# Optimization experiments

Measured on AMD Instinct MI355X. Metric: run time of the kernel, lower is better.

The kernel has to match this reference:

```python
import jax, jax.numpy as jnp
import numpy as np

N_LIG, N_REC = 4096, 16384
E_LIG, E_REC = 65536, 262144
H, OUT, ORIG = 256, 256, 64
EF_LIG, EF_REC = 16, 16
N_SIG = 15
SLOPE = 0.01      # leakyrelu_neg_slope
SKIP_H = 0.5      # skip_weight_h
X_INIT = 0.25     # x_connection_init
SIGMAS = np.asarray(1.5 ** np.arange(N_SIG), dtype=np.float32)  # all_sigmas_dist


def _lrelu(x):
    return jax.nn.leaky_relu(x, SLOPE)


def _mlp2(x, w1, b1, w2, b2):
    # Linear -> LeakyReLU -> (Identity norm) -> Linear
    return _lrelu(x @ w1 + b1) @ w2 + b2


def _seg_mean(vals, idx, n):
    s = jax.ops.segment_sum(vals, idx, num_segments=n)
    d = jax.ops.segment_sum(jnp.ones((vals.shape[0], 1), vals.dtype), idx, num_segments=n)
    return s / jnp.maximum(d, 1.0)


def _rbf(x_rel):
    # multi-sigma RBF of squared edge distance: exp(-|x_rel|^2 / sigma), 15 sigmas
    d2 = jnp.sum(x_rel * x_rel, axis=1, keepdims=True)        # [E,1]
    return jnp.exp(-d2 / jnp.asarray(SIGMAS, x_rel.dtype))    # [E,15]


def _cross_attention(q, k, v, mask):
    a = mask * (q @ k.T) - 1000.0 * (1.0 - mask)
    return jax.nn.softmax(a, axis=1) @ v


def setup_inputs():
    key = jax.random.key(0)
    ks = iter(jax.random.split(key, 64))

    def rn(*shape):
        return jax.random.normal(next(ks), shape, dtype=jnp.float32)

    def w(fi, fo):
        return rn(fi, fo) / np.float32(np.sqrt(fi))

    e_in_l = 2 * H + EF_LIG + N_SIG
    e_in_r = 2 * H + EF_REC + N_SIG
    n_in = ORIG + H + OUT
    z = lambda d: jnp.zeros((d,), jnp.float32)
    inp = dict(
        coords_lig=rn(N_LIG, 3), h_feats_lig=rn(N_LIG, H),
        orig_lig_feats=rn(N_LIG, ORIG), orig_coords_lig=rn(N_LIG, 3),
        coords_rec=rn(N_REC, 3), h_feats_rec=rn(N_REC, H),
        orig_rec_feats=rn(N_REC, ORIG), orig_coords_rec=rn(N_REC, 3),
        mask=jnp.ones((N_LIG, N_REC), jnp.float32),
        lig_edge_feat=rn(E_LIG, EF_LIG), rec_edge_feat=rn(E_REC, EF_REC),
        lig_src=jax.random.randint(next(ks), (E_LIG,), 0, N_LIG),
        lig_dst=jax.random.randint(next(ks), (E_LIG,), 0, N_LIG),
        rec_src=jax.random.randint(next(ks), (E_REC,), 0, N_REC),
        rec_dst=jax.random.randint(next(ks), (E_REC,), 0, N_REC),
        lig_edge_w1=w(e_in_l, OUT), lig_edge_b1=z(OUT), lig_edge_w2=w(OUT, OUT), lig_edge_b2=z(OUT),
        rec_edge_w1=w(e_in_r, OUT), rec_edge_b1=z(OUT), rec_edge_w2=w(OUT, OUT), rec_edge_b2=z(OUT),
        att_q_lig_w=w(H, H), att_k_lig_w=w(H, H), att_v_lig_w=w(H, H),
        att_q_rec_w=w(H, H), att_k_rec_w=w(H, H), att_v_rec_w=w(H, H),
        node_lig_w1=w(n_in, H), node_lig_b1=z(H), node_lig_w2=w(H, OUT), node_lig_b2=z(OUT),
        node_rec_w1=w(n_in, H), node_rec_b1=z(H), node_rec_w2=w(H, OUT), node_rec_b2=z(OUT),
        coords_lig_w1=w(OUT, OUT), coords_lig_b1=z(OUT), coords_lig_w2=w(OUT, 1), coords_lig_b2=z(1),
        coords_rec_w1=w(OUT, OUT), coords_rec_b1=z(OUT), coords_rec_w2=w(OUT, 1), coords_rec_b2=z(1),
    )
    return inp


def reference(coords_lig, h_feats_lig, orig_lig_feats, orig_coords_lig,
              coords_rec, h_feats_rec, orig_rec_feats, orig_coords_rec,
              mask, lig_edge_feat, rec_edge_feat,
              lig_src, lig_dst, rec_src, rec_dst,
              lig_edge_w1, lig_edge_b1, lig_edge_w2, lig_edge_b2,
              rec_edge_w1, rec_edge_b1, rec_edge_w2, rec_edge_b2,
              att_q_lig_w, att_k_lig_w, att_v_lig_w,
              att_q_rec_w, att_k_rec_w, att_v_rec_w,
              node_lig_w1, node_lig_b1, node_lig_w2, node_lig_b2,
              node_rec_w1, node_rec_b1, node_rec_w2, node_rec_b2,
              coords_lig_w1, coords_lig_b1, coords_lig_w2, coords_lig_b2,
              coords_rec_w1, coords_rec_b1, coords_rec_w2, coords_rec_b2):
    n_lig, n_rec = coords_lig.shape[0], coords_rec.shape[0]
    # edge messages: gather endpoint features + edge attrs + RBF(dist)
    x_rel_l = coords_lig[lig_src] - coords_lig[lig_dst]                       # [E_lig,3]
    msg_l = _mlp2(jnp.concatenate([h_feats_lig[lig_src], h_feats_lig[lig_dst],
                                   lig_edge_feat, _rbf(x_rel_l)], axis=1),
                  lig_edge_w1, lig_edge_b1, lig_edge_w2, lig_edge_b2)         # [E_lig,OUT]
    x_rel_r = coords_rec[rec_src] - coords_rec[rec_dst]
    msg_r = _mlp2(jnp.concatenate([h_feats_rec[rec_src], h_feats_rec[rec_dst],
                                   rec_edge_feat, _rbf(x_rel_r)], axis=1),
                  rec_edge_w1, rec_edge_b1, rec_edge_w2, rec_edge_b2)         # [E_rec,OUT]
    # cross attention between ligand and receptor node sets
    cross_l = _cross_attention(_lrelu(h_feats_lig @ att_q_lig_w),
                               _lrelu(h_feats_rec @ att_k_rec_w),
                               h_feats_rec @ att_v_rec_w, mask)               # [N_lig,H]
    cross_r = _cross_attention(_lrelu(h_feats_rec @ att_q_rec_w),
                               _lrelu(h_feats_lig @ att_k_lig_w),
                               h_feats_lig @ att_v_lig_w, mask.T)             # [N_rec,H]
    # equivariant coordinate updates: mean over incoming edges of x_rel * coords_mlp(msg)
    x_upd_l = _seg_mean(x_rel_l * _mlp2(msg_l, coords_lig_w1, coords_lig_b1,
                                        coords_lig_w2, coords_lig_b2), lig_dst, n_lig)
    x_upd_r = _seg_mean(x_rel_r * _mlp2(msg_r, coords_rec_w1, coords_rec_b1,
                                        coords_rec_w2, coords_rec_b2), rec_dst, n_rec)
    x_ev_l = X_INIT * orig_coords_lig + (1.0 - X_INIT) * coords_lig + x_upd_l
    x_ev_r = X_INIT * orig_coords_rec + (1.0 - X_INIT) * coords_rec + x_upd_r
    # node feature updates: cat(aggr_msg, cross_att, original features) -> MLP + skip
    aggr_l = _seg_mean(msg_l, lig_dst, n_lig)
    aggr_r = _seg_mean(msg_r, rec_dst, n_rec)
    h_l = SKIP_H * _mlp2(jnp.concatenate([aggr_l, cross_l, orig_lig_feats], axis=1),
                         node_lig_w1, node_lig_b1, node_lig_w2, node_lig_b2) \
          + (1.0 - SKIP_H) * h_feats_lig
    h_r = SKIP_H * _mlp2(jnp.concatenate([aggr_r, cross_r, orig_rec_feats], axis=1),
                         node_rec_w1, node_rec_b1, node_rec_w2, node_rec_b2) \
          + (1.0 - SKIP_H) * h_feats_rec
    return (x_ev_l, h_l, x_ev_r, h_r)
```

## Files before the change

### kernel.cpp

```cpp
#include <hip/hip_runtime.h>
#include <hip/hip_bf16.h>


#define N_LIG   4096
#define N_REC   16384
#define E_LIG_N 65536
#define E_REC_N 262144
#define HD      256
#define ORIGD   64
#define EFD     16
#define NSIG    15
#define EIN     543
#define XP      552
#define XPN     584
#define XPP     264
#define FP      264

typedef __bf16 bf16x8 __attribute__((ext_vector_type(8)));
typedef float  f32x4  __attribute__((ext_vector_type(4)));

__device__ __forceinline__ float lrelu(float x) { return x > 0.f ? x : 0.01f * x; }
__device__ __forceinline__ unsigned short f2bu(float f) {
    __hip_bfloat16 h = __float2bfloat16(f);
    return *reinterpret_cast<unsigned short*>(&h);
}

__device__ __forceinline__ void glds16(const void* g, void* l) {
    __builtin_amdgcn_global_load_lds(
        (const __attribute__((address_space(1))) void*)g,
        (__attribute__((address_space(3))) void*)l,
        16, 0, 0);
}

__device__ __forceinline__ void stage_tile(
    const __hip_bfloat16* g, unsigned short* l, int wave, int lane)
{
    #pragma unroll
    for (int i = 0; i < 2; ++i) {
        const __hip_bfloat16* gp = g + (size_t)(i * 512 + wave * 64 + lane) * 8;
        unsigned short* lp = l + (i * 512 + wave * 64) * 8;
        glds16(gp, lp);
    }
}

__device__ __forceinline__ void mfma_gemm(
    const unsigned short* sA, int pitch,
    const __hip_bfloat16* Wswz, int KS, int lane, f32x4 acc[2][4])
{
    const int col = lane & 15, quad = lane >> 4;
    const unsigned short* a0p = sA + (size_t)col * pitch + quad * 8;
    const unsigned short* a1p = sA + (size_t)(16 + col) * pitch + quad * 8;
    const __hip_bfloat16* wp = Wswz + lane * 8;
    bf16x8 bc[4], bn[4], a0c, a1c, a0n, a1n;
    #pragma unroll
    for (int nt = 0; nt < 4; ++nt)
        bc[nt] = *reinterpret_cast<const bf16x8*>(wp + (size_t)nt * KS * 512);
    a0c = *reinterpret_cast<const bf16x8*>(a0p);
    a1c = *reinterpret_cast<const bf16x8*>(a1p);
    for (int ks = 0; ks < KS; ++ks) {
        if (ks + 1 < KS) {
            #pragma unroll
            for (int nt = 0; nt < 4; ++nt)
                bn[nt] = *reinterpret_cast<const bf16x8*>(
                    wp + ((size_t)nt * KS + ks + 1) * 512);
            a0n = *reinterpret_cast<const bf16x8*>(a0p + (ks + 1) * 32);
            a1n = *reinterpret_cast<const bf16x8*>(a1p + (ks + 1) * 32);
        }
        #pragma unroll
        for (int nt = 0; nt < 4; ++nt) {
            acc[0][nt] = __builtin_amdgcn_mfma_f32_16x16x32_bf16(a0c, bc[nt], acc[0][nt], 0, 0, 0);
            acc[1][nt] = __builtin_amdgcn_mfma_f32_16x16x32_bf16(a1c, bc[nt], acc[1][nt], 0, 0, 0);
        }
        #pragma unroll
        for (int nt = 0; nt < 4; ++nt) bc[nt] = bn[nt];
        a0c = a0n; a1c = a1n;
    }
}

__global__ void zero_kernel(float* __restrict__ p, int n) {
    int i = blockIdx.x * 256 + threadIdx.x;
    if (i < n) p[i] = 0.f;
}

__global__ void f2b_kernel(const float* __restrict__ src,
                           __hip_bfloat16* __restrict__ dst, int n8) {
    const int i = blockIdx.x * 256 + threadIdx.x;
    if (i >= n8) return;
    const float4 a = *reinterpret_cast<const float4*>(src + (size_t)i * 8);
    const float4 b = *reinterpret_cast<const float4*>(src + (size_t)i * 8 + 4);
    ushort4 u0 = { f2bu(a.x), f2bu(a.y), f2bu(a.z), f2bu(a.w) };
    ushort4 u1 = { f2bu(b.x), f2bu(b.y), f2bu(b.z), f2bu(b.w) };
    unsigned short* d = (unsigned short*)dst + (size_t)i * 8;
    *reinterpret_cast<ushort4*>(d)     = u0;
    *reinterpret_cast<ushort4*>(d + 4) = u1;
}

__global__ void hist_kernel(const int* __restrict__ dst, int* __restrict__ hist, int n) {
    int i = blockIdx.x * 256 + threadIdx.x;
    if (i < n) atomicAdd(&hist[dst[i]], 1);
}

__global__ __launch_bounds__(256) void scan_kernel(
    const int* __restrict__ hist, int* __restrict__ cur,
    float* __restrict__ cntf, int n)
{
    __shared__ int part[256];
    const int tid = threadIdx.x;
    const int per = n >> 8;
    const int base = tid * per;
    int s = 0;
    for (int i = 0; i < per; ++i) s += hist[base + i];
    part[tid] = s;
    __syncthreads();
    #pragma unroll
    for (int off = 1; off < 256; off <<= 1) {
        int v = (tid >= off) ? part[tid - off] : 0;
        __syncthreads();
        part[tid] += v;
        __syncthreads();
    }
    int run = part[tid] - s;
    for (int i = 0; i < per; ++i) {
        const int h = hist[base + i];
        cur[base + i]  = run;
        cntf[base + i] = (float)h;
        run += h;
    }
}

__global__ void scatter_kernel(const int* __restrict__ dst, int* __restrict__ cur,
                               int* __restrict__ elist, int n) {
    int i = blockIdx.x * 256 + threadIdx.x;
    if (i < n) { int p = atomicAdd(&cur[dst[i]], 1); elist[p] = i; }
}

__global__ void wt_swz(const float* __restrict__ src,
                       __hip_bfloat16* __restrict__ dst, int K, int KS) {
    const int g  = blockIdx.x / KS;
    const int ks = blockIdx.x % KS;
    for (int i = threadIdx.x; i < 512; i += 256) {
        const int lane = i >> 3, j = i & 7;
        const int n = g * 16 + (lane & 15);
        const int k = ks * 32 + (lane >> 4) * 8 + j;
        const float v = (k < K) ? src[(size_t)k * 256 + n] : 0.f;
        dst[((size_t)(g * KS + ks) * 64 + lane) * 8 + j] = __float2bfloat16(v);
    }
}

__global__ __launch_bounds__(256) void kswz_kernel(
    const __hip_bfloat16* __restrict__ K, __hip_bfloat16* __restrict__ blob)
{
    const int c = blockIdx.x * 256 + threadIdx.x;
    const int lane = c & 63;
    const int s    = (c >> 6) & 7;
    const int kt   = c >> 9;
    const __hip_bfloat16* src =
        K + (size_t)(kt * 16 + (lane & 15)) * HD + s * 32 + (lane >> 4) * 8;
    *reinterpret_cast<uint4*>(blob + (size_t)c * 8) =
        *reinterpret_cast<const uint4*>(src);
}

__global__ __launch_bounds__(256) void vswz_kernel(
    const __hip_bfloat16* __restrict__ V, __hip_bfloat16* __restrict__ blob)
{
    __shared__ unsigned short s[32][264];
    const int jt  = blockIdx.x;
    const int tid = threadIdx.x;
    {
        const int row = tid >> 3;
        const int d0  = (tid & 7) * 32;
        const __hip_bfloat16* vp = V + (size_t)(jt * 32 + row) * HD + d0;
        #pragma unroll
        for (int i = 0; i < 4; ++i)
            *reinterpret_cast<uint4*>(&s[row][d0 + 8 * i]) =
                *reinterpret_cast<const uint4*>(vp + 8 * i);
    }
    __syncthreads();
    {
        const int w    = tid >> 6;
        const int lane = tid & 63;
        const int col  = lane & 15;
        const int quad = lane >> 4;
        #pragma unroll
        for (int i = 0; i < 4; ++i) {
            const int dt = w + i * 4;
            unsigned short tmp[8];
            #pragma unroll
            for (int j = 0; j < 8; ++j)
                tmp[j] = s[quad * 8 + j][dt * 16 + col];
            *reinterpret_cast<uint4*>(
                blob + ((size_t)(jt * 16 + dt) * 64 + lane) * 8) =
                *reinterpret_cast<uint4*>(tmp);
        }
    }
}

__global__ __launch_bounds__(256, 4) void edge_mfma(
    const float* __restrict__ coords, const __hip_bfloat16* __restrict__ hb,
    const __hip_bfloat16* __restrict__ efb,
    const int* __restrict__ src, const int* __restrict__ dst,
    const int* __restrict__ elist,
    const __hip_bfloat16* __restrict__ W1s, const float* __restrict__ b1,
    const __hip_bfloat16* __restrict__ W2s, const float* __restrict__ b2,
    const __hip_bfloat16* __restrict__ Wc1s, const float* __restrict__ bc1,
    const float* __restrict__ wc2v, const float* __restrict__ bc2,
    float* __restrict__ aggr, float* __restrict__ xsum)
{
    __shared__ unsigned short sX[32][XP];
    __shared__ float sXrel[32][3];
    __shared__ int   sDst[32];
    __shared__ int   sSrc[32];
    __shared__ int   sE[32];
    __shared__ float sRedW[4][32];
    __shared__ float sPv[32];

    const int tid  = threadIdx.x;
    const int lane = tid & 63;
    const int wave = tid >> 6;
    const int col  = lane & 15;
    const int quad = lane >> 4;
    const int e0   = blockIdx.x * 32;

    if (tid < 32) {
        const int e = elist[e0 + tid];
        const int s = src[e], d = dst[e];
        sE[tid] = e; sSrc[tid] = s; sDst[tid] = d;
        float d2 = 0.f;
        #pragma unroll
        for (int c = 0; c < 3; ++c) {
            const float xr = coords[s * 3 + c] - coords[d * 3 + c];
            sXrel[tid][c] = xr;
            d2 += xr * xr;
        }
        float sig = 1.0f;
        #pragma unroll
        for (int si = 0; si < NSIG; ++si) {
            sX[tid][528 + si] = f2bu(__expf(-d2 / sig));
            sig *= 1.5f;
        }
        sX[tid][543] = 0;
    }
    __syncthreads();

    for (int i = tid; i < 32 * 64; i += 256) {
        const int row = i >> 6, c = i & 63;
        const int node = (c < 32) ? sSrc[row] : sDst[row];
        const int chunk = c & 31;
        *reinterpret_cast<uint4*>(&sX[row][(c < 32 ? 0 : 256) + chunk * 8]) =
            *reinterpret_cast<const uint4*>(&hb[(size_t)node * HD + chunk * 8]);
    }
    if (tid < 64) {
        const int row = tid >> 1, hh = tid & 1;
        *reinterpret_cast<uint4*>(&sX[row][512 + hh * 8]) =
            *reinterpret_cast<const uint4*>(&efb[(size_t)sE[row] * EFD + hh * 8]);
    }
    __syncthreads();

    f32x4 acc[2][4];
    f32x4 macc[2][4];

    #pragma unroll
    for (int nt = 0; nt < 4; ++nt) {
        const float bv = b1[wave * 64 + nt * 16 + col];
        acc[0][nt] = { bv, bv, bv, bv };
        acc[1][nt] = { bv, bv, bv, bv };
    }
    mfma_gemm(&sX[0][0], XP, W1s + (size_t)(wave * 4) * 17 * 512, 17, lane, acc);
    __syncthreads();
    #pragma unroll
    for (int mt = 0; mt < 2; ++mt)
        #pragma unroll
        for (int nt = 0; nt < 4; ++nt)
            #pragma unroll
            for (int r = 0; r < 4; ++r)
                sX[mt * 16 + quad * 4 + r][wave * 64 + nt * 16 + col] =
                    f2bu(lrelu(acc[mt][nt][r]));
    __syncthreads();

    #pragma unroll
    for (int nt = 0; nt < 4; ++nt) {
        const float bv = b2[wave * 64 + nt * 16 + col];
        macc[0][nt] = { bv, bv, bv, bv };
        macc[1][nt] = { bv, bv, bv, bv };
    }
    mfma_gemm(&sX[0][0], XP, W2s + (size_t)(wave * 4) * 8 * 512, 8, lane, macc);
    __syncthreads();
    #pragma unroll
    for (int mt = 0; mt < 2; ++mt)
        #pragma unroll
        for (int nt = 0; nt < 4; ++nt)
            #pragma unroll
            for (int r = 0; r < 4; ++r)
                sX[mt * 16 + quad * 4 + r][wave * 64 + nt * 16 + col] =
                    f2bu(macc[mt][nt][r]);
    __syncthreads();

    #pragma unroll
    for (int nt = 0; nt < 4; ++nt) {
        const float bv = bc1[wave * 64 + nt * 16 + col];
        acc[0][nt] = { bv, bv, bv, bv };
        acc[1][nt] = { bv, bv, bv, bv };
    }
    mfma_gemm(&sX[0][0], XP, Wc1s + (size_t)(wave * 4) * 8 * 512, 8, lane, acc);
    float w2l[4];
    #pragma unroll
    for (int nt = 0; nt < 4; ++nt) w2l[nt] = wc2v[wave * 64 + nt * 16 + col];
    #pragma unroll
    for (int mt = 0; mt < 2; ++mt) {
        float pr[4] = { 0.f, 0.f, 0.f, 0.f };
        #pragma unroll
        for (int nt = 0; nt < 4; ++nt)
            #pragma unroll
            for (int r = 0; r < 4; ++r)
                pr[r] += lrelu(acc[mt][nt][r]) * w2l[nt];
        #pragma unroll
        for (int r = 0; r < 4; ++r) {
            #pragma unroll
            for (int off = 1; off < 16; off <<= 1) pr[r] += __shfl_xor(pr[r], off);
        }
        if (col == 0)
            #pragma unroll
            for (int r = 0; r < 4; ++r)
                sRedW[wave][mt * 16 + quad * 4 + r] = pr[r];
    }
    __syncthreads();

    float* sF = reinterpret_cast<float*>(&sX[0][0]);
    #pragma unroll
    for (int mt = 0; mt < 2; ++mt)
        #pragma unroll
        for (int nt = 0; nt < 4; ++nt)
            #pragma unroll
            for (int r = 0; r < 4; ++r)
                sF[(mt * 16 + quad * 4 + r) * FP + wave * 64 + nt * 16 + col] =
                    macc[mt][nt][r];
    if (tid < 32)
        sPv[tid] = sRedW[0][tid] + sRedW[1][tid] + sRedW[2][tid] + sRedW[3][tid]
                 + bc2[0];
    __syncthreads();

    {
        const int c = tid;
        float av = 0.f;
        int dprev = sDst[0];
        for (int row = 0; row < 32; ++row) {
            const int d = sDst[row];
            if (d != dprev) {
                atomicAdd(&aggr[(size_t)dprev * HD + c], av);
                av = 0.f; dprev = d;
            }
            av += sF[row * FP + c];
        }
        atomicAdd(&aggr[(size_t)dprev * HD + c], av);
    }
    if (tid < 3) {
        const int c = tid;
        float av = 0.f;
        int dprev = sDst[0];
        for (int row = 0; row < 32; ++row) {
            const int d = sDst[row];
            if (d != dprev) {
                atomicAdd(&xsum[(size_t)dprev * 3 + c], av);
                av = 0.f; dprev = d;
            }
            av += sXrel[row][c] * sPv[row];
        }
        atomicAdd(&xsum[(size_t)dprev * 3 + c], av);
    }
}

__global__ __launch_bounds__(256, 4) void node_mfma(
    const float* __restrict__ aggr, const float* __restrict__ cnt,
    const __hip_bfloat16* __restrict__ cross, const float* __restrict__ orig,
    const float* __restrict__ hfeat,
    const __hip_bfloat16* __restrict__ WN1s, const float* __restrict__ b1,
    const __hip_bfloat16* __restrict__ WN2s, const float* __restrict__ b2,
    float* __restrict__ out)
{
    __shared__ unsigned short sXn[32][XPN];
    __shared__ float sInv[32];

    const int tid  = threadIdx.x;
    const int lane = tid & 63;
    const int wave = tid >> 6;
    const int col  = lane & 15;
    const int quad = lane >> 4;
    const int r0   = blockIdx.x * 32;

    if (tid < 32) sInv[tid] = 1.f / fmaxf(cnt[r0 + tid], 1.f);
    __syncthreads();

    for (int i = tid; i < 32 * 64; i += 256) {
        const int row = i >> 6, c4 = i & 63;
        const float inv = sInv[row];
        const float4 v = *reinterpret_cast<const float4*>(
            &aggr[(size_t)(r0 + row) * HD + c4 * 4]);
        ushort4 u = { f2bu(v.x * inv), f2bu(v.y * inv), f2bu(v.z * inv), f2bu(v.w * inv) };
        *reinterpret_cast<ushort4*>(&sXn[row][c4 * 4]) = u;
    }
    for (int i = tid; i < 32 * 64; i += 256) {
        const int row = i >> 6, c4 = i & 63;
        const ushort4 u = *reinterpret_cast<const ushort4*>(
            &cross[(size_t)(r0 + row) * HD + c4 * 4]);
        *reinterpret_cast<ushort4*>(&sXn[row][256 + c4 * 4]) = u;
    }
    for (int i = tid; i < 32 * 16; i += 256) {
        const int row = i >> 4, c4 = i & 15;
        const float4 v = *reinterpret_cast<const float4*>(
            &orig[(size_t)(r0 + row) * ORIGD + c4 * 4]);
        ushort4 u = { f2bu(v.x), f2bu(v.y), f2bu(v.z), f2bu(v.w) };
        *reinterpret_cast<ushort4*>(&sXn[row][512 + c4 * 4]) = u;
    }
    __syncthreads();

    f32x4 acc[2][4];

    #pragma unroll
    for (int nt = 0; nt < 4; ++nt) {
        const float bv = b1[wave * 64 + nt * 16 + col];
        acc[0][nt] = { bv, bv, bv, bv };
        acc[1][nt] = { bv, bv, bv, bv };
    }
    mfma_gemm(&sXn[0][0], XPN, WN1s + (size_t)(wave * 4) * 18 * 512, 18, lane, acc);
    __syncthreads();
    #pragma unroll
    for (int mt = 0; mt < 2; ++mt)
        #pragma unroll
        for (int nt = 0; nt < 4; ++nt)
            #pragma unroll
            for (int r = 0; r < 4; ++r)
                sXn[mt * 16 + quad * 4 + r][wave * 64 + nt * 16 + col] =
                    f2bu(lrelu(acc[mt][nt][r]));
    __syncthreads();

    #pragma unroll
    for (int nt = 0; nt < 4; ++nt) {
        const float bv = b2[wave * 64 + nt * 16 + col];
        acc[0][nt] = { bv, bv, bv, bv };
        acc[1][nt] = { bv, bv, bv, bv };
    }
    mfma_gemm(&sXn[0][0], XPN, WN2s + (size_t)(wave * 4) * 8 * 512, 8, lane, acc);
    #pragma unroll
    for (int mt = 0; mt < 2; ++mt)
        #pragma unroll
        for (int nt = 0; nt < 4; ++nt)
            #pragma unroll
            for (int r = 0; r < 4; ++r) {
                const int g = r0 + mt * 16 + quad * 4 + r;
                const int n = wave * 64 + nt * 16 + col;
                out[(size_t)g * HD + n] =
                    0.5f * acc[mt][nt][r] + 0.5f * hfeat[(size_t)g * HD + n];
            }
}

__global__ __launch_bounds__(256, 4) void qkv_proj(
    const __hip_bfloat16* __restrict__ Xb,
    const __hip_bfloat16* __restrict__ Wq, const __hip_bfloat16* __restrict__ Wk,
    const __hip_bfloat16* __restrict__ Wv,
    __hip_bfloat16* __restrict__ Q, __hip_bfloat16* __restrict__ K,
    __hip_bfloat16* __restrict__ V)
{
    __shared__ unsigned short sXp[32][XPP];
    const int tid  = threadIdx.x;
    const int lane = tid & 63;
    const int wave = tid >> 6;
    const int col  = lane & 15;
    const int quad = lane >> 4;
    const int r0   = blockIdx.x * 32;

    for (int i = tid; i < 32 * 32; i += 256) {
        const int row = i >> 5, c = i & 31;
        *reinterpret_cast<uint4*>(&sXp[row][c * 8]) =
            *reinterpret_cast<const uint4*>(&Xb[(size_t)(r0 + row) * HD + c * 8]);
    }
    __syncthreads();

    f32x4 acc[2][4];
    #pragma unroll
    for (int p = 0; p < 3; ++p) {
        const __hip_bfloat16* Ws = (p == 0) ? Wq : (p == 1) ? Wk : Wv;
        __hip_bfloat16* outp     = (p == 0) ? Q  : (p == 1) ? K  : V;
        #pragma unroll
        for (int nt = 0; nt < 4; ++nt) {
            acc[0][nt] = { 0.f, 0.f, 0.f, 0.f };
            acc[1][nt] = { 0.f, 0.f, 0.f, 0.f };
        }
        mfma_gemm(&sXp[0][0], XPP, Ws + (size_t)(wave * 4) * 8 * 512, 8, lane, acc);
        #pragma unroll
        for (int mt = 0; mt < 2; ++mt)
            #pragma unroll
            for (int nt = 0; nt < 4; ++nt)
                #pragma unroll
                for (int r = 0; r < 4; ++r) {
                    float v = acc[mt][nt][r];
                    if (p < 2) v = lrelu(v);
                    outp[(size_t)(r0 + mt * 16 + quad * 4 + r) * HD +
                         wave * 64 + nt * 16 + col] = __float2bfloat16(v);
                }
    }
}

__device__ __forceinline__ void load_mask(
    const float* __restrict__ maskG, int transposed, int R0, int j0,
    int wave, int quad, int col, float mv[2][4])
{
    if (!transposed) {
        #pragma unroll
        for (int t = 0; t < 2; ++t)
            #pragma unroll
            for (int r = 0; r < 4; ++r)
                mv[t][r] = maskG[(size_t)(R0 + wave * 16 + quad * 4 + r) * N_REC
                                 + j0 + col + 16 * t];
    } else {
        #pragma unroll
        for (int t = 0; t < 2; ++t)
            #pragma unroll
            for (int r = 0; r < 4; ++r)
                mv[t][r] = maskG[(size_t)(j0 + col + 16 * t) * N_REC
                                 + R0 + wave * 16 + quad * 4 + r];
    }
}

__device__ __forceinline__ void attn_tile(
    const unsigned short* sK, const unsigned short* sV,
    unsigned short (*sPw)[40], const bf16x8 qf[8], const float mv[2][4],
    int lane, int col, int quad, f32x4 o[16], float m[4], float l[4])
{
    f32x4 sacc[2];
    sacc[0][0]=0.f; sacc[0][1]=0.f; sacc[0][2]=0.f; sacc[0][3]=0.f;
    sacc[1][0]=0.f; sacc[1][1]=0.f; sacc[1][2]=0.f; sacc[1][3]=0.f;
    #pragma unroll
    for (int t = 0; t < 2; ++t) {
        #pragma unroll
        for (int s = 0; s < 8; ++s) {
            bf16x8 kf = *reinterpret_cast<const bf16x8*>(
                &sK[(t * 8 + s) * 512 + lane * 8]);
            sacc[t] = __builtin_amdgcn_mfma_f32_16x16x32_bf16(qf[s], kf, sacc[t], 0, 0, 0);
        }
    }

    float a[2][4];
    #pragma unroll
    for (int t = 0; t < 2; ++t)
        #pragma unroll
        for (int r = 0; r < 4; ++r)
            a[t][r] = mv[t][r] * sacc[t][r] - 1000.f * (1.f - mv[t][r]);

    float lm[4];
    #pragma unroll
    for (int r = 0; r < 4; ++r) lm[r] = fmaxf(a[0][r], a[1][r]);
    float w = lm[0] - m[0];
    #pragma unroll
    for (int r = 1; r < 4; ++r) w = fmaxf(w, lm[r] - m[r]);
    if (!__all(w <= 8.f)) {
        #pragma unroll
        for (int r = 0; r < 4; ++r) {
            float mx = lm[r];
            #pragma unroll
            for (int off = 1; off < 16; off <<= 1)
                mx = fmaxf(mx, __shfl_xor(mx, off));
            const float mn = fmaxf(m[r], mx);
            const float c  = __expf(m[r] - mn);
            m[r] = mn;
            l[r] *= c;
            #pragma unroll
            for (int dt = 0; dt < 16; ++dt) o[dt][r] *= c;
        }
    }

    #pragma unroll
    for (int r = 0; r < 4; ++r) {
        const float p0 = __expf(a[0][r] - m[r]);
        const float p1 = __expf(a[1][r] - m[r]);
        sPw[quad * 4 + r][col]      = f2bu(p0);
        sPw[quad * 4 + r][col + 16] = f2bu(p1);
        l[r] += p0 + p1;
    }

    bf16x8 pf = *reinterpret_cast<const bf16x8*>(&sPw[col][quad * 8]);
    #pragma unroll
    for (int dt = 0; dt < 16; ++dt) {
        bf16x8 vf = *reinterpret_cast<const bf16x8*>(&sV[dt * 512 + lane * 8]);
        o[dt] = __builtin_amdgcn_mfma_f32_16x16x32_bf16(pf, vf, o[dt], 0, 0, 0);
    }
}

__global__ __launch_bounds__(512) void attn_mfma(
    const __hip_bfloat16* __restrict__ Qb, const __hip_bfloat16* __restrict__ Kz,
    const __hip_bfloat16* __restrict__ Vz, const float* __restrict__ maskG,
    float* __restrict__ PO, float* __restrict__ PM, float* __restrict__ PL,
    int M, int chunkKeys, int transposed)
{
    __shared__ unsigned short sKb[2][8192];
    __shared__ unsigned short sVb[2][8192];
    __shared__ unsigned short sP[8][16][40];

    const int tid  = threadIdx.x;
    const int lane = tid & 63;
    const int wave = tid >> 6;
    const int col  = lane & 15;
    const int quad = lane >> 4;
    const int R0   = blockIdx.x * 128;
    const int split = blockIdx.y;
    const int jbase = split * chunkKeys;

    bf16x8 qf[8];
    {
        const __hip_bfloat16* qp =
            Qb + (size_t)(R0 + wave * 16 + col) * HD + quad * 8;
        #pragma unroll
        for (int s = 0; s < 8; ++s)
            qf[s] = *reinterpret_cast<const bf16x8*>(qp + 32 * s);
    }

    f32x4 o[16];
    #pragma unroll
    for (int dt = 0; dt < 16; ++dt) { o[dt][0]=0.f; o[dt][1]=0.f; o[dt][2]=0.f; o[dt][3]=0.f; }
    float m[4], l[4];
    #pragma unroll
    for (int r = 0; r < 4; ++r) { m[r] = -INFINITY; l[r] = 0.f; }

    float mvA[2][4], mvB[2][4];

    stage_tile(Kz + (size_t)jbase * 256, &sKb[0][0], wave, lane);
    stage_tile(Vz + (size_t)jbase * 256, &sVb[0][0], wave, lane);
    load_mask(maskG, transposed, R0, jbase, wave, quad, col, mvA);

    for (int jt = 0; jt < chunkKeys; jt += 64) {
        asm volatile("s_waitcnt vmcnt(0)" ::: "memory");
        __builtin_amdgcn_s_barrier();
        __builtin_amdgcn_sched_barrier(0);
        stage_tile(Kz + (size_t)(jbase + jt + 32) * 256, &sKb[1][0], wave, lane);
        stage_tile(Vz + (size_t)(jbase + jt + 32) * 256, &sVb[1][0], wave, lane);
        load_mask(maskG, transposed, R0, jbase + jt + 32, wave, quad, col, mvB);
        __builtin_amdgcn_sched_barrier(0);
        attn_tile(&sKb[0][0], &sVb[0][0], sP[wave], qf, mvA,
                  lane, col, quad, o, m, l);

        asm volatile("s_waitcnt vmcnt(0)" ::: "memory");
        __builtin_amdgcn_s_barrier();
        __builtin_amdgcn_sched_barrier(0);
        if (jt + 64 < chunkKeys) {
            stage_tile(Kz + (size_t)(jbase + jt + 64) * 256, &sKb[0][0], wave, lane);
            stage_tile(Vz + (size_t)(jbase + jt + 64) * 256, &sVb[0][0], wave, lane);
            load_mask(maskG, transposed, R0, jbase + jt + 64, wave, quad, col, mvA);
        }
        __builtin_amdgcn_sched_barrier(0);
        attn_tile(&sKb[1][0], &sVb[1][0], sP[wave], qf, mvB,
                  lane, col, quad, o, m, l);
    }

    #pragma unroll
    for (int r = 0; r < 4; ++r) {
        #pragma unroll
        for (int off = 1; off < 16; off <<= 1)
            l[r] += __shfl_xor(l[r], off);
    }

    #pragma unroll
    for (int dt = 0; dt < 16; ++dt)
        #pragma unroll
        for (int r = 0; r < 4; ++r) {
            const int row = R0 + wave * 16 + quad * 4 + r;
            PO[((size_t)split * M + row) * HD + dt * 16 + col] = o[dt][r];
        }
    if (col == 0) {
        #pragma unroll
        for (int r = 0; r < 4; ++r) {
            const int row = R0 + wave * 16 + quad * 4 + r;
            PM[(size_t)split * M + row] = m[r];
            PL[(size_t)split * M + row] = l[r];
        }
    }
}

__global__ void attn_combine(
    const float* __restrict__ PO, const float* __restrict__ PM,
    const float* __restrict__ PL, __hip_bfloat16* __restrict__ Out,
    int M, int nchunks)
{
    const int idx = blockIdx.x * 256 + threadIdx.x;
    const int row = idx >> 8;
    float mmax = -INFINITY;
    for (int c = 0; c < nchunks; ++c) mmax = fmaxf(mmax, PM[(size_t)c * M + row]);
    float denom = 0.f, acc = 0.f;
    for (int c = 0; c < nchunks; ++c) {
        const float w = __expf(PM[(size_t)c * M + row] - mmax);
        denom += PL[(size_t)c * M + row] * w;
        acc   += PO[(size_t)c * M * HD + idx] * w;
    }
    Out[idx] = __float2bfloat16(acc / denom);
}

__global__ void coords_fin(
    const float* __restrict__ coords, const float* __restrict__ origc,
    const float* __restrict__ xsum, const float* __restrict__ cnt,
    float* __restrict__ out, int n)
{
    const int i = blockIdx.x * 256 + threadIdx.x;
    if (i >= n * 3) return;
    const int node = i / 3;
    const float inv = 1.f / fmaxf(cnt[node], 1.f);
    out[i] = 0.25f * origc[i] + 0.75f * coords[i] + xsum[i] * inv;
}

extern "C" void kernel_launch(void* const* d_in, const int* in_sizes, int n_in,
                              void* d_out, int out_size, void* d_ws, size_t ws_size,
                              hipStream_t stream)
{
    const float* coords_lig = (const float*)d_in[0];
    const float* h_lig      = (const float*)d_in[1];
    const float* orig_lig   = (const float*)d_in[2];
    const float* origc_lig  = (const float*)d_in[3];
    const float* coords_rec = (const float*)d_in[4];
    const float* h_rec      = (const float*)d_in[5];
    const float* orig_rec   = (const float*)d_in[6];
    const float* origc_rec  = (const float*)d_in[7];
    const float* mask       = (const float*)d_in[8];
    const float* lig_ef     = (const float*)d_in[9];
    const float* rec_ef     = (const float*)d_in[10];
    const int* lig_src = (const int*)d_in[11];
    const int* lig_dst = (const int*)d_in[12];
    const int* rec_src = (const int*)d_in[13];
    const int* rec_dst = (const int*)d_in[14];
    const float* le_w1 = (const float*)d_in[15];
    const float* le_b1 = (const float*)d_in[16];
    const float* le_w2 = (const float*)d_in[17];
    const float* le_b2 = (const float*)d_in[18];
    const float* re_w1 = (const float*)d_in[19];
    const float* re_b1 = (const float*)d_in[20];
    const float* re_w2 = (const float*)d_in[21];
    const float* re_b2 = (const float*)d_in[22];
    const float* aql_w = (const float*)d_in[23];
    const float* akl_w = (const float*)d_in[24];
    const float* avl_w = (const float*)d_in[25];
    const float* aqr_w = (const float*)d_in[26];
    const float* akr_w = (const float*)d_in[27];
    const float* avr_w = (const float*)d_in[28];
    const float* nl_w1 = (const float*)d_in[29];
    const float* nl_b1 = (const float*)d_in[30];
    const float* nl_w2 = (const float*)d_in[31];
    const float* nl_b2 = (const float*)d_in[32];
    const float* nr_w1 = (const float*)d_in[33];
    const float* nr_b1 = (const float*)d_in[34];
    const float* nr_w2 = (const float*)d_in[35];
    const float* nr_b2 = (const float*)d_in[36];
    const float* cl_w1 = (const float*)d_in[37];
    const float* cl_b1 = (const float*)d_in[38];
    const float* cl_w2 = (const float*)d_in[39];
    const float* cl_b2 = (const float*)d_in[40];
    const float* cr_w1 = (const float*)d_in[41];
    const float* cr_b1 = (const float*)d_in[42];
    const float* cr_w2 = (const float*)d_in[43];
    const float* cr_b2 = (const float*)d_in[44];

    float* out = (float*)d_out;
    float* wsf = (float*)d_ws;

    const size_t AGGRL = 0;
    const size_t AGGRR = AGGRL + (size_t)N_LIG * HD;
    const size_t CNTL  = AGGRR + (size_t)N_REC * HD;
    const size_t CNTR  = CNTL + N_LIG;
    const size_t XSUML = CNTR + N_REC;
    const size_t XSUMR = XSUML + (size_t)N_LIG * 3;
    const size_t HISTL = XSUMR + (size_t)N_REC * 3;
    const size_t CURL  = HISTL + N_LIG;
    const size_t HISTR = CURL + N_LIG;
    const size_t CURR  = HISTR + N_REC;
    const size_t ZEND  = CURR + N_REC;
    const size_t ELISTL = ZEND;
    const size_t ELISTR = ELISTL + E_LIG_N;
    const size_t FEND   = ELISTR + E_REC_N;

    __hip_bfloat16* wsb = (__hip_bfloat16*)(wsf + FEND);
    const size_t QL  = 0;
    const size_t KL  = QL + (size_t)N_LIG * HD;
    const size_t VL  = KL + (size_t)N_LIG * HD;
    const size_t QR  = VL + (size_t)N_LIG * HD;
    const size_t KR  = QR + (size_t)N_REC * HD;
    const size_t VR  = KR + (size_t)N_REC * HD;
    const size_t CRL = VR + (size_t)N_REC * HD;
    const size_t CRR = CRL + (size_t)N_LIG * HD;
    const size_t KZL = CRR + (size_t)N_REC * HD;
    const size_t VZL = KZL + (size_t)N_LIG * HD;
    const size_t KZR = VZL + (size_t)N_LIG * HD;
    const size_t VZR = KZR + (size_t)N_REC * HD;
    const size_t EW1SZ = (size_t)16 * 17 * 512;
    const size_t KW256 = (size_t)16 * 8 * 512;
    const size_t NW1SZ = (size_t)16 * 18 * 512;
    const size_t SW_EL1 = VZR + (size_t)N_REC * HD;
    const size_t SW_EL2 = SW_EL1 + EW1SZ;
    const size_t SW_EC1 = SW_EL2 + KW256;
    const size_t SW_NL1 = SW_EC1 + KW256;
    const size_t SW_NL2 = SW_NL1 + NW1SZ;
    const size_t SW_ER1 = SW_NL2 + KW256;
    const size_t SW_ER2 = SW_ER1 + EW1SZ;
    const size_t SW_EC1R = SW_ER2 + KW256;
    const size_t SW_NR1 = SW_EC1R + KW256;
    const size_t SW_NR2 = SW_NR1 + NW1SZ;
    const size_t SW_PQL = SW_NR2 + KW256;
    const size_t SW_PKL = SW_PQL + KW256;
    const size_t SW_PVL = SW_PKL + KW256;
    const size_t SW_PQR = SW_PVL + KW256;
    const size_t SW_PKR = SW_PQR + KW256;
    const size_t SW_PVR = SW_PKR + KW256;
    const size_t HB_L  = SW_PVR + KW256;
    const size_t HB_R  = HB_L + (size_t)N_LIG * HD;
    const size_t EFB_L = HB_R + (size_t)N_REC * HD;
    const size_t EFB_R = EFB_L + (size_t)E_LIG_N * EFD;
    const size_t BF_END = EFB_R + (size_t)E_REC_N * EFD;

    float* wsp = (float*)(wsb + ((BF_END + 1) & ~(size_t)1));
    const size_t baseBytes = (size_t)((char*)wsp - (char*)d_ws);
    int SL = 16, SR = 4;
    {
        const size_t poElems16 = (size_t)16 * N_LIG * HD;
        const size_t need16 = baseBytes +
            (poElems16 + 2 * (size_t)16 * N_LIG) * sizeof(float);
        if (ws_size < need16) { SL = 8; SR = 2; }
    }
    const size_t PO_ = 0;
    const size_t PM_ = PO_ + (size_t)SL * N_LIG * HD;
    const size_t PL_ = PM_ + (size_t)SL * N_LIG;

    const size_t O_XL = 0;
    const size_t O_HL = O_XL + (size_t)N_LIG * 3;
    const size_t O_XR = O_HL + (size_t)N_LIG * HD;
    const size_t O_HR = O_XR + (size_t)N_REC * 3;

    zero_kernel<<<((int)ZEND + 255) / 256, 256, 0, stream>>>(wsf, (int)ZEND);

    f2b_kernel<<<(N_LIG * HD / 8 + 255) / 256, 256, 0, stream>>>(
        h_lig, wsb + HB_L, N_LIG * HD / 8);
    f2b_kernel<<<(N_REC * HD / 8 + 255) / 256, 256, 0, stream>>>(
        h_rec, wsb + HB_R, N_REC * HD / 8);
    f2b_kernel<<<(E_LIG_N * EFD / 8 + 255) / 256, 256, 0, stream>>>(
        lig_ef, wsb + EFB_L, E_LIG_N * EFD / 8);
    f2b_kernel<<<(E_REC_N * EFD / 8 + 255) / 256, 256, 0, stream>>>(
        rec_ef, wsb + EFB_R, E_REC_N * EFD / 8);

    hist_kernel<<<E_LIG_N / 256, 256, 0, stream>>>(lig_dst, (int*)(wsf + HISTL), E_LIG_N);
    hist_kernel<<<E_REC_N / 256, 256, 0, stream>>>(rec_dst, (int*)(wsf + HISTR), E_REC_N);
    scan_kernel<<<1, 256, 0, stream>>>((int*)(wsf + HISTL), (int*)(wsf + CURL),
                                       wsf + CNTL, N_LIG);
    scan_kernel<<<1, 256, 0, stream>>>((int*)(wsf + HISTR), (int*)(wsf + CURR),
                                       wsf + CNTR, N_REC);
    scatter_kernel<<<E_LIG_N / 256, 256, 0, stream>>>(
        lig_dst, (int*)(wsf + CURL), (int*)(wsf + ELISTL), E_LIG_N);
    scatter_kernel<<<E_REC_N / 256, 256, 0, stream>>>(
        rec_dst, (int*)(wsf + CURR), (int*)(wsf + ELISTR), E_REC_N);

    wt_swz<<<16 * 17, 256, 0, stream>>>(le_w1, wsb + SW_EL1, EIN, 17);
    wt_swz<<<16 * 8,  256, 0, stream>>>(le_w2, wsb + SW_EL2, 256, 8);
    wt_swz<<<16 * 8,  256, 0, stream>>>(cl_w1, wsb + SW_EC1, 256, 8);
    wt_swz<<<16 * 18, 256, 0, stream>>>(nl_w1, wsb + SW_NL1, 576, 18);
    wt_swz<<<16 * 8,  256, 0, stream>>>(nl_w2, wsb + SW_NL2, 256, 8);
    wt_swz<<<16 * 17, 256, 0, stream>>>(re_w1, wsb + SW_ER1, EIN, 17);
    wt_swz<<<16 * 8,  256, 0, stream>>>(re_w2, wsb + SW_ER2, 256, 8);
    wt_swz<<<16 * 8,  256, 0, stream>>>(cr_w1, wsb + SW_EC1R, 256, 8);
    wt_swz<<<16 * 18, 256, 0, stream>>>(nr_w1, wsb + SW_NR1, 576, 18);
    wt_swz<<<16 * 8,  256, 0, stream>>>(nr_w2, wsb + SW_NR2, 256, 8);
    wt_swz<<<16 * 8,  256, 0, stream>>>(aql_w, wsb + SW_PQL, 256, 8);
    wt_swz<<<16 * 8,  256, 0, stream>>>(akl_w, wsb + SW_PKL, 256, 8);
    wt_swz<<<16 * 8,  256, 0, stream>>>(avl_w, wsb + SW_PVL, 256, 8);
    wt_swz<<<16 * 8,  256, 0, stream>>>(aqr_w, wsb + SW_PQR, 256, 8);
    wt_swz<<<16 * 8,  256, 0, stream>>>(akr_w, wsb + SW_PKR, 256, 8);
    wt_swz<<<16 * 8,  256, 0, stream>>>(avr_w, wsb + SW_PVR, 256, 8);

    edge_mfma<<<E_LIG_N / 32, 256, 0, stream>>>(
        coords_lig, wsb + HB_L, wsb + EFB_L, lig_src, lig_dst,
        (const int*)(wsf + ELISTL),
        wsb + SW_EL1, le_b1, wsb + SW_EL2, le_b2, wsb + SW_EC1, cl_b1, cl_w2, cl_b2,
        wsf + AGGRL, wsf + XSUML);
    edge_mfma<<<E_REC_N / 32, 256, 0, stream>>>(
        coords_rec, wsb + HB_R, wsb + EFB_R, rec_src, rec_dst,
        (const int*)(wsf + ELISTR),
        wsb + SW_ER1, re_b1, wsb + SW_ER2, re_b2, wsb + SW_EC1R, cr_b1, cr_w2, cr_b2,
        wsf + AGGRR, wsf + XSUMR);

    qkv_proj<<<N_LIG / 32, 256, 0, stream>>>(
        wsb + HB_L, wsb + SW_PQL, wsb + SW_PKL, wsb + SW_PVL,
        wsb + QL, wsb + KL, wsb + VL);
    qkv_proj<<<N_REC / 32, 256, 0, stream>>>(
        wsb + HB_R, wsb + SW_PQR, wsb + SW_PKR, wsb + SW_PVR,
        wsb + QR, wsb + KR, wsb + VR);
    kswz_kernel<<<N_LIG / 8, 256, 0, stream>>>(wsb + KL, wsb + KZL);
    kswz_kernel<<<N_REC / 8, 256, 0, stream>>>(wsb + KR, wsb + KZR);
    vswz_kernel<<<N_LIG / 32, 256, 0, stream>>>(wsb + VL, wsb + VZL);
    vswz_kernel<<<N_REC / 32, 256, 0, stream>>>(wsb + VR, wsb + VZR);

    {
        dim3 gl(N_LIG / 128, SL);
        attn_mfma<<<gl, 512, 0, stream>>>(wsb + QL, wsb + KZR, wsb + VZR, mask,
                                          wsp + PO_, wsp + PM_, wsp + PL_,
                                          N_LIG, N_REC / SL, 0);
        attn_combine<<<N_LIG, 256, 0, stream>>>(
            wsp + PO_, wsp + PM_, wsp + PL_, wsb + CRL, N_LIG, SL);

        dim3 gr(N_REC / 128, SR);
        attn_mfma<<<gr, 512, 0, stream>>>(wsb + QR, wsb + KZL, wsb + VZL, mask,
                                          wsp + PO_, wsp + PM_, wsp + PL_,
                                          N_REC, N_LIG / SR, 1);
        attn_combine<<<N_REC, 256, 0, stream>>>(
            wsp + PO_, wsp + PM_, wsp + PL_, wsb + CRR, N_REC, SR);
    }

    coords_fin<<<(N_LIG * 3 + 255) / 256, 256, 0, stream>>>(
        coords_lig, origc_lig, wsf + XSUML, wsf + CNTL, out + O_XL, N_LIG);
    coords_fin<<<(N_REC * 3 + 255) / 256, 256, 0, stream>>>(
        coords_rec, origc_rec, wsf + XSUMR, wsf + CNTR, out + O_XR, N_REC);

    node_mfma<<<N_LIG / 32, 256, 0, stream>>>(
        wsf + AGGRL, wsf + CNTL, wsb + CRL, orig_lig, h_lig,
        wsb + SW_NL1, nl_b1, wsb + SW_NL2, nl_b2, out + O_HL);
    node_mfma<<<N_REC / 32, 256, 0, stream>>>(
        wsf + AGGRR, wsf + CNTR, wsb + CRR, orig_rec, h_rec,
        wsb + SW_NR1, nr_b1, wsb + SW_NR2, nr_b2, out + O_HR);

    (void)in_sizes; (void)n_in; (void)out_size;
}
```

Before: 1.312 ms.

## Write swizzled K/V directly from QKV projection and unroll MFMA k-loop by two

The QKV projection now writes K and V straight into the MFMA-swizzled layouts the attention kernel reads, so the separate K/V swizzle kernels and their extra global read/write passes go away. The shared GEMM helper is also restructured into an even/odd double-buffered loop that removes the register copies between iterations. The trade-off is that the swizzled stores from the projection are scattered, so they may coalesce worse than the old row-major writes.

```diff
diff --git a/kernel.cpp b/kernel.cpp
--- a/kernel.cpp
+++ b/kernel.cpp
@@ -51,29 +51,53 @@
     const unsigned short* a0p = sA + (size_t)col * pitch + quad * 8;
     const unsigned short* a1p = sA + (size_t)(16 + col) * pitch + quad * 8;
     const __hip_bfloat16* wp = Wswz + lane * 8;
-    bf16x8 bc[4], bn[4], a0c, a1c, a0n, a1n;
-    #pragma unroll
-    for (int nt = 0; nt < 4; ++nt)
-        bc[nt] = *reinterpret_cast<const bf16x8*>(wp + (size_t)nt * KS * 512);
-    a0c = *reinterpret_cast<const bf16x8*>(a0p);
-    a1c = *reinterpret_cast<const bf16x8*>(a1p);
-    for (int ks = 0; ks < KS; ++ks) {
-        if (ks + 1 < KS) {
+
+    bf16x8 bE[4], bO[4], aE0, aE1, aO0, aO1;
+    #pragma unroll
+    for (int nt = 0; nt < 4; ++nt) {
+        bE[nt] = *reinterpret_cast<const bf16x8*>(wp + (size_t)nt * KS * 512);
+        bO[nt] = *reinterpret_cast<const bf16x8*>(wp + ((size_t)nt * KS + 1) * 512);
+    }
+    aE0 = *reinterpret_cast<const bf16x8*>(a0p);
+    aE1 = *reinterpret_cast<const bf16x8*>(a1p);
+    aO0 = *reinterpret_cast<const bf16x8*>(a0p + 32);
+    aO1 = *reinterpret_cast<const bf16x8*>(a1p + 32);
+
+    int ks = 0;
+    for (; ks + 2 <= KS; ks += 2) {
+        #pragma unroll
+        for (int nt = 0; nt < 4; ++nt) {
+            acc[0][nt] = __builtin_amdgcn_mfma_f32_16x16x32_bf16(aE0, bE[nt], acc[0][nt], 0, 0, 0);
+            acc[1][nt] = __builtin_amdgcn_mfma_f32_16x16x32_bf16(aE1, bE[nt], acc[1][nt], 0, 0, 0);
+        }
+        if (ks + 2 < KS) {
             #pragma unroll
             for (int nt = 0; nt < 4; ++nt)
-                bn[nt] = *reinterpret_cast<const bf16x8*>(
-                    wp + ((size_t)nt * KS + ks + 1) * 512);
-            a0n = *reinterpret_cast<const bf16x8*>(a0p + (ks + 1) * 32);
-            a1n = *reinterpret_cast<const bf16x8*>(a1p + (ks + 1) * 32);
+                bE[nt] = *reinterpret_cast<const bf16x8*>(
+                    wp + ((size_t)nt * KS + ks + 2) * 512);
+            aE0 = *reinterpret_cast<const bf16x8*>(a0p + (ks + 2) * 32);
+            aE1 = *reinterpret_cast<const bf16x8*>(a1p + (ks + 2) * 32);
         }
         #pragma unroll
         for (int nt = 0; nt < 4; ++nt) {
-            acc[0][nt] = __builtin_amdgcn_mfma_f32_16x16x32_bf16(a0c, bc[nt], acc[0][nt], 0, 0, 0);
-            acc[1][nt] = __builtin_amdgcn_mfma_f32_16x16x32_bf16(a1c, bc[nt], acc[1][nt], 0, 0, 0);
-        }
-        #pragma unroll
-        for (int nt = 0; nt < 4; ++nt) bc[nt] = bn[nt];
-        a0c = a0n; a1c = a1n;
+            acc[0][nt] = __builtin_amdgcn_mfma_f32_16x16x32_bf16(aO0, bO[nt], acc[0][nt], 0, 0, 0);
+            acc[1][nt] = __builtin_amdgcn_mfma_f32_16x16x32_bf16(aO1, bO[nt], acc[1][nt], 0, 0, 0);
+        }
+        if (ks + 3 < KS) {
+            #pragma unroll
+            for (int nt = 0; nt < 4; ++nt)
+                bO[nt] = *reinterpret_cast<const bf16x8*>(
+                    wp + ((size_t)nt * KS + ks + 3) * 512);
+            aO0 = *reinterpret_cast<const bf16x8*>(a0p + (ks + 3) * 32);
+            aO1 = *reinterpret_cast<const bf16x8*>(a1p + (ks + 3) * 32);
+        }
+    }
+    if (ks < KS) {
+        #pragma unroll
+        for (int nt = 0; nt < 4; ++nt) {
+            acc[0][nt] = __builtin_amdgcn_mfma_f32_16x16x32_bf16(aE0, bE[nt], acc[0][nt], 0, 0, 0);
+            acc[1][nt] = __builtin_amdgcn_mfma_f32_16x16x32_bf16(aE1, bE[nt], acc[1][nt], 0, 0, 0);
+        }
     }
 }
 
@@ -147,54 +171,6 @@
     }
 }
 
-__global__ __launch_bounds__(256) void kswz_kernel(
-    const __hip_bfloat16* __restrict__ K, __hip_bfloat16* __restrict__ blob)
-{
-    const int c = blockIdx.x * 256 + threadIdx.x;
-    const int lane = c & 63;
-    const int s    = (c >> 6) & 7;
-    const int kt   = c >> 9;
-    const __hip_bfloat16* src =
-        K + (size_t)(kt * 16 + (lane & 15)) * HD + s * 32 + (lane >> 4) * 8;
-    *reinterpret_cast<uint4*>(blob + (size_t)c * 8) =
-        *reinterpret_cast<const uint4*>(src);
-}
-
-__global__ __launch_bounds__(256) void vswz_kernel(
-    const __hip_bfloat16* __restrict__ V, __hip_bfloat16* __restrict__ blob)
-{
-    __shared__ unsigned short s[32][264];
-    const int jt  = blockIdx.x;
-    const int tid = threadIdx.x;
-    {
-        const int row = tid >> 3;
-        const int d0  = (tid & 7) * 32;
-        const __hip_bfloat16* vp = V + (size_t)(jt * 32 + row) * HD + d0;
-        #pragma unroll
-        for (int i = 0; i < 4; ++i)
-            *reinterpret_cast<uint4*>(&s[row][d0 + 8 * i]) =
-                *reinterpret_cast<const uint4*>(vp + 8 * i);
-    }
-    __syncthreads();
-    {
-        const int w    = tid >> 6;
-        const int lane = tid & 63;
-        const int col  = lane & 15;
-        const int quad = lane >> 4;
-        #pragma unroll
-        for (int i = 0; i < 4; ++i) {
-            const int dt = w + i * 4;
-            unsigned short tmp[8];
-            #pragma unroll
-            for (int j = 0; j < 8; ++j)
-                tmp[j] = s[quad * 8 + j][dt * 16 + col];
-            *reinterpret_cast<uint4*>(
-                blob + ((size_t)(jt * 16 + dt) * 64 + lane) * 8) =
-                *reinterpret_cast<uint4*>(tmp);
-        }
-    }
-}
-
 __global__ __launch_bounds__(256, 4) void edge_mfma(
     const float* __restrict__ coords, const __hip_bfloat16* __restrict__ hb,
     const __hip_bfloat16* __restrict__ efb,
@@ -457,8 +433,8 @@
     const __hip_bfloat16* __restrict__ Xb,
     const __hip_bfloat16* __restrict__ Wq, const __hip_bfloat16* __restrict__ Wk,
     const __hip_bfloat16* __restrict__ Wv,
-    __hip_bfloat16* __restrict__ Q, __hip_bfloat16* __restrict__ K,
-    __hip_bfloat16* __restrict__ V)
+    __hip_bfloat16* __restrict__ Q, __hip_bfloat16* __restrict__ Kz,
+    __hip_bfloat16* __restrict__ Vz)
 {
     __shared__ unsigned short sXp[32][XPP];
     const int tid  = threadIdx.x;
@@ -479,7 +455,6 @@
     #pragma unroll
     for (int p = 0; p < 3; ++p) {
         const __hip_bfloat16* Ws = (p == 0) ? Wq : (p == 1) ? Wk : Wv;
-        __hip_bfloat16* outp     = (p == 0) ? Q  : (p == 1) ? K  : V;
         #pragma unroll
         for (int nt = 0; nt < 4; ++nt) {
             acc[0][nt] = { 0.f, 0.f, 0.f, 0.f };
@@ -493,9 +468,21 @@
                 #pragma unroll
                 for (int r = 0; r < 4; ++r) {
                     float v = acc[mt][nt][r];
-                    if (p < 2) v = lrelu(v);
-                    outp[(size_t)(r0 + mt * 16 + quad * 4 + r) * HD +
-                         wave * 64 + nt * 16 + col] = __float2bfloat16(v);
+                    const int row = r0 + mt * 16 + quad * 4 + r;
+                    const int c   = wave * 64 + nt * 16 + col;
+                    if (p == 0) {
+                        Q[(size_t)row * HD + c] = __float2bfloat16(lrelu(v));
+                    } else if (p == 1) {
+                        const int kt = row >> 4, rr = row & 15;
+                        const int s  = c >> 5, cc8 = (c >> 3) & 3, j = c & 7;
+                        Kz[(size_t)(kt * 8 + s) * 512 + (cc8 * 16 + rr) * 8 + j] =
+                            __float2bfloat16(lrelu(v));
+                    } else {
+                        const int jt = row >> 5, rowin = row & 31;
+                        const int dt = c >> 4, cc = c & 15;
+                        Vz[((size_t)(jt * 16 + dt) * 64 + (rowin >> 3) * 16 + cc) * 8
+                           + (rowin & 7)] = __float2bfloat16(v);
+                    }
                 }
     }
 }
@@ -880,14 +867,10 @@
 
     qkv_proj<<<N_LIG / 32, 256, 0, stream>>>(
         wsb + HB_L, wsb + SW_PQL, wsb + SW_PKL, wsb + SW_PVL,
-        wsb + QL, wsb + KL, wsb + VL);
+        wsb + QL, wsb + KZL, wsb + VZL);
     qkv_proj<<<N_REC / 32, 256, 0, stream>>>(
         wsb + HB_R, wsb + SW_PQR, wsb + SW_PKR, wsb + SW_PVR,
-        wsb + QR, wsb + KR, wsb + VR);
-    kswz_kernel<<<N_LIG / 8, 256, 0, stream>>>(wsb + KL, wsb + KZL);
-    kswz_kernel<<<N_REC / 8, 256, 0, stream>>>(wsb + KR, wsb + KZR);
-    vswz_kernel<<<N_LIG / 32, 256, 0, stream>>>(wsb + VL, wsb + VZL);
-    vswz_kernel<<<N_REC / 32, 256, 0, stream>>>(wsb + VR, wsb + VZR);
+        wsb + QR, wsb + KZR, wsb + VZR);
 
     {
         dim3 gl(N_LIG / 128, SL);
```

Measured after the change: 1.299 ms, median of 2. Within noise of the previous version (-1.0%).
